# Performance work log

Measured on AMD Instinct MI355X. Metric: run time of the kernel, lower is better.

The kernel has to match this reference:

```python
import jax, jax.numpy as jnp
import numpy as np

B, L, T, V = 64, 512, 1000, 256
E, H, M, S = 256, 512, 80, 128  # text_embed, hidden, n_mels, speaker_dim


def lstm_scan(x, Wih, Whh, b):
    # x: [T, B, D]; torch gate order i, f, g, o; bias = b_ih + b_hh fused
    Bn = x.shape[1]
    Hn = Whh.shape[1]
    h0 = jnp.zeros((Bn, Hn), x.dtype)

    def step(carry, xt):
        h, c = carry
        g = xt @ Wih.T + h @ Whh.T + b
        i, f, gg, o = jnp.split(g, 4, axis=-1)
        c = jax.nn.sigmoid(f) * c + jax.nn.sigmoid(i) * jnp.tanh(gg)
        h = jax.nn.sigmoid(o) * jnp.tanh(c)
        return (h, c), h

    _, ys = jax.lax.scan(step, (h0, h0), x)
    return ys  # [T, B, H]


def setup_inputs() -> dict:
    key = jax.random.key(0)
    ks = jax.random.split(key, 32)
    r = lambda i, shp: (jax.random.normal(ks[i], shp, jnp.float32) * 0.1)
    Hd = H // 2  # 256, per-direction biLSTM hidden
    inp = {
        "text_input": jax.random.randint(ks[0], (B, L), 0, V),
        "speaker_embedding": jax.random.normal(ks[1], (B, S), jnp.float32),
        "target_mel": jax.random.normal(ks[2], (B, T, M), jnp.float32),
        "embed": r(3, (V, E)),
        # bidirectional text LSTM (hidden//2 per direction)
        "enc_Wih_f": r(4, (4 * Hd, E)), "enc_Whh_f": r(5, (4 * Hd, Hd)), "enc_b_f": r(6, (4 * Hd,)),
        "enc_Wih_b": r(7, (4 * Hd, E)), "enc_Whh_b": r(8, (4 * Hd, Hd)), "enc_b_b": r(9, (4 * Hd,)),
        # speaker projection MLP
        "sp_W1": r(10, (H, S)), "sp_b1": r(11, (H,)),
        "sp_W2": r(12, (H, H)), "sp_b2": r(13, (H,)),
        # 2-layer decoder LSTM, input = H + M = 592
        "dec_Wih0": r(14, (4 * H, H + M)), "dec_Whh0": r(15, (4 * H, H)), "dec_b0": r(16, (4 * H,)),
        "dec_Wih1": r(17, (4 * H, H)), "dec_Whh1": r(18, (4 * H, H)), "dec_b1": r(19, (4 * H,)),
        # mel projection MLP
        "mel_W1": r(20, (H, H)), "mel_b1": r(21, (H,)),
        "mel_W2": r(22, (M, H)), "mel_b2": r(23, (M,)),
        # stop token projection
        "stop_W": r(24, (1, H)), "stop_b": r(25, (1,)),
    }
    return inp


def reference(text_input, speaker_embedding, target_mel, embed,
              enc_Wih_f, enc_Whh_f, enc_b_f, enc_Wih_b, enc_Whh_b, enc_b_b,
              sp_W1, sp_b1, sp_W2, sp_b2,
              dec_Wih0, dec_Whh0, dec_b0, dec_Wih1, dec_Whh1, dec_b1,
              mel_W1, mel_b1, mel_W2, mel_b2, stop_W, stop_b):
    # --- text encoder: embedding + biLSTM ---
    x = jnp.swapaxes(embed[text_input], 0, 1)  # [L, B, E]
    fwd = lstm_scan(x, enc_Wih_f, enc_Whh_f, enc_b_f)          # [L, B, H/2]
    bwd = lstm_scan(x[::-1], enc_Wih_b, enc_Whh_b, enc_b_b)[::-1]
    text_encoded = jnp.swapaxes(jnp.concatenate([fwd, bwd], -1), 0, 1)  # [B, L, H]

    # --- speaker projection, broadcast over text length ---
    sp = jax.nn.relu(speaker_embedding @ sp_W1.T + sp_b1) @ sp_W2.T + sp_b2  # [B, H]
    encoder_output = text_encoded + sp[:, None, :]  # [B, L, H]

    # --- teacher-forced decoder: query_t = encoder_output[:, t % L] ---
    idx = jnp.arange(T) % L
    query = encoder_output[:, idx]  # [B, T, H]
    dec_mel_in = jnp.concatenate(
        [jnp.zeros((B, 1, M), target_mel.dtype), target_mel[:, :-1]], axis=1)  # [B, T, M]
    rnn_in = jnp.swapaxes(jnp.concatenate([dec_mel_in, query], -1), 0, 1)  # [T, B, H+M]

    h1 = lstm_scan(rnn_in, dec_Wih0, dec_Whh0, dec_b0)  # [T, B, H]
    h2 = lstm_scan(h1, dec_Wih1, dec_Whh1, dec_b1)      # [T, B, H]
    out = jnp.swapaxes(h2, 0, 1)  # [B, T, H]

    mel_outputs = jax.nn.relu(out @ mel_W1.T + mel_b1) @ mel_W2.T + mel_b2  # [B, T, M]
    stop_outputs = out @ stop_W.T + stop_b  # [B, T, 1]
    return mel_outputs, stop_outputs
```

## Files before the change

### kernel.cpp

```cpp
#include <hip/hip_runtime.h>
#include <cstdint>
#include <cstddef>


#define DEVI __device__ __forceinline__

typedef short bf16x8 __attribute__((ext_vector_type(8)));
typedef float f32x4 __attribute__((ext_vector_type(4)));
typedef unsigned short u16x4 __attribute__((ext_vector_type(4)));

constexpr int B_ = 64, L_ = 512, T_ = 1000, E_ = 256, H_ = 512, M_ = 80, S_ = 128, Hd_ = 256;

DEVI unsigned short f2bs(float f) {
  unsigned u = __builtin_bit_cast(unsigned, f);
  unsigned r = u + 0x7fffu + ((u >> 16) & 1u);
  return (unsigned short)(r >> 16);
}
DEVI float b2f(unsigned short s) { return __builtin_bit_cast(float, (unsigned)s << 16); }
DEVI void split2(float v, unsigned short& hi, unsigned short& lo) {
  hi = f2bs(v);
  lo = f2bs(v - b2f(hi));
}
DEVI float sigm(float x) { x = fminf(fmaxf(x, -30.f), 30.f); return 1.f / (1.f + __expf(-x)); }
DEVI float tanh_(float x) { x = fminf(fmaxf(x, -15.f), 15.f); float e = __expf(2.f * x); return (e - 1.f) / (e + 1.f); }

DEVI f32x4 mfma16(bf16x8 a, bf16x8 b, f32x4 c) {
  return __builtin_amdgcn_mfma_f32_16x16x32_bf16(a, b, c, 0, 0, 0);
}

DEVI void ldc16(bf16x8& r, const unsigned short* p) {
  asm volatile("global_load_dwordx4 %0, %1, off sc0 sc1" : "=v"(r) : "v"(p));
}
DEVI void st4c(unsigned short* p, unsigned v) {
  asm volatile("global_store_dword %0, %1, off sc0 sc1" :: "v"(p), "v"(v));
}
DEVI void st8c(unsigned short* p, u16x4 v) {
  asm volatile("global_store_dwordx2 %0, %1, off sc0 sc1" :: "v"(p), "v"(v));
}
DEVI int pollld(const int* p) {
  int v;
  asm volatile("global_load_dword %0, %1, off sc0 sc1\ns_waitcnt vmcnt(0)"
               : "=v"(v) : "v"(p) : "memory");
  return v;
}
#define VM_DRAIN() do { asm volatile("s_waitcnt vmcnt(0)" ::: "memory"); \
                        __builtin_amdgcn_sched_barrier(0); } while (0)
#define VM_WAIT8_OR_0(LAST) do { \
    if (LAST) asm volatile("s_waitcnt vmcnt(0)" ::: "memory"); \
    else      asm volatile("s_waitcnt vmcnt(8)" ::: "memory"); \
    __builtin_amdgcn_sched_barrier(0); } while (0)

struct Bar { int sub[8][64]; int master[64]; int release[64]; };

DEVI void grid_bar(Bar* bb, int nwg, int step) {
  __syncthreads();
  if (threadIdx.x == 0) {
    const int per = nwg >> 3;
    int old = __hip_atomic_fetch_add(&bb->sub[blockIdx.x & 7][0], 1,
                                     __ATOMIC_RELAXED, __HIP_MEMORY_SCOPE_AGENT);
    if (old == per * (step + 1) - 1) {
      int om = __hip_atomic_fetch_add(&bb->master[0], 1,
                                      __ATOMIC_RELAXED, __HIP_MEMORY_SCOPE_AGENT);
      if (om == 8 * (step + 1) - 1)
        __hip_atomic_fetch_add(&bb->release[0], 1,
                               __ATOMIC_RELAXED, __HIP_MEMORY_SCOPE_AGENT);
    }
    while (pollld(&bb->release[0]) < step + 1) __builtin_amdgcn_s_sleep(1);
  }
  __syncthreads();
}

__global__ void k_prep(const float* __restrict__ embed, const float* __restrict__ tmel,
                       const float* __restrict__ mw1, const float* __restrict__ mw2,
                       unsigned short* emb_h, unsigned short* emb_l,
                       unsigned short* mel_h, unsigned short* mel_l,
                       unsigned short* w1_bf, unsigned short* w2_bf) {
  const long long stride = (long long)gridDim.x * blockDim.x;
  const long long i0 = (long long)blockIdx.x * blockDim.x + threadIdx.x;
  for (long long i = i0; i < 256 * 256; i += stride) {
    unsigned short h, l; split2(embed[i], h, l);
    emb_h[i] = h; emb_l[i] = l;
  }
  for (long long i = i0; i < (long long)T_ * B_ * 96; i += stride) {
    int c = (int)(i % 96);
    long long tb = i / 96;
    int b = (int)(tb % B_);
    int t = (int)(tb / B_);
    float v = 0.f;
    if (t > 0 && c < 80) v = tmel[((long long)b * T_ + (t - 1)) * M_ + c];
    unsigned short h, l; split2(v, h, l);
    mel_h[i] = h; mel_l[i] = l;
  }
  for (long long i = i0; i < 512 * 512; i += stride) w1_bf[i] = f2bs(mw1[i]);
  for (long long i = i0; i < 80 * 512; i += stride) w2_bf[i] = f2bs(mw2[i]);
}

__global__ void __launch_bounds__(512) k_sp(const float* __restrict__ spk,
                                            const float* __restrict__ w1, const float* __restrict__ b1,
                                            const float* __restrict__ w2, const float* __restrict__ b2,
                                            float* sp) {
  __shared__ float t1[512];
  const int b = blockIdx.x, j = threadIdx.x;
  float a = b1[j];
  const float* sr = spk + b * S_;
  for (int k = 0; k < S_; ++k) a += sr[k] * w1[j * S_ + k];
  t1[j] = fmaxf(a, 0.f);
  __syncthreads();
  float a2 = b2[j];
  for (int k = 0; k < H_; ++k) a2 += t1[k] * w2[j * H_ + k];
  sp[b * H_ + j] = a2;
}

constexpr int ENC_LDS = 2 * 16 * 4 * 64 * 16 + 4 * 64 * 16 * 4 + 256;

__global__ void __launch_bounds__(256) k_enc(
    const int* __restrict__ text,
    const float* __restrict__ WihF, const float* __restrict__ WhhF, const float* __restrict__ bF,
    const float* __restrict__ WihB, const float* __restrict__ WhhB, const float* __restrict__ bB,
    const unsigned short* __restrict__ emb_h, const unsigned short* __restrict__ emb_l,
    const float* __restrict__ sp,
    unsigned short* hencfh, unsigned short* hencfl,
    unsigned short* ench, unsigned short* encl, Bar* bar) {
  extern __shared__ char lds[];
  unsigned short* Wh = (unsigned short*)lds;
  unsigned short* Wl = Wh + 16 * 4 * 64 * 8;
  float* G = (float*)(lds + 2 * 16 * 4 * 64 * 16);
  float* bias = G + 4 * 64 * 16;

  const int wg = blockIdx.x;
  const int dir = wg >> 4;
  const int jhb = (wg & 15) * 16;
  const int tid = threadIdx.x;
  const int wv = tid >> 6, ln = tid & 63, lg = ln >> 4, lr = ln & 15;

  const float* Wih = dir ? WihB : WihF;
  const float* Whh = dir ? WhhB : WhhF;
  const float* bb = dir ? bB : bF;

  for (int s = tid; s < 16 * 4 * 64; s += 256) {
    int kb = s >> 8, g = (s >> 6) & 3, l = s & 63;
    int R = g * Hd_ + jhb + (l & 15);
    int k0 = kb * 32 + (l >> 4) * 8;
    const float* src = (k0 < E_) ? (Wih + (size_t)R * E_ + k0) : (Whh + (size_t)R * Hd_ + (k0 - E_));
    bf16x8 vh, vl;
#pragma unroll
    for (int j = 0; j < 8; ++j) {
      unsigned short a, b; split2(src[j], a, b);
      vh[j] = (short)a; vl[j] = (short)b;
    }
    *(bf16x8*)(Wh + (size_t)s * 8) = vh;
    *(bf16x8*)(Wl + (size_t)s * 8) = vl;
  }
  if (tid < 64) bias[tid] = bb[(tid >> 4) * Hd_ + jhb + (tid & 15)];

  const int eb = tid >> 2, ej0 = (tid & 3) * 4;
  float c4[4] = {0.f, 0.f, 0.f, 0.f};
  float spv[4];
#pragma unroll
  for (int q = 0; q < 4; ++q) spv[q] = sp[eb * H_ + dir * Hd_ + jhb + ej0 + q];

  const int jh = jhb + ej0;
  const size_t fro = ((size_t)((jh >> 5) * 4 + (eb >> 4)) * 64 +
                      (((jh >> 3) & 3) * 16 + (eb & 15))) * 8 + (jh & 7);

  __syncthreads();

  for (int t = 0; t < L_; ++t) {
    const int tpos = dir ? (L_ - 1 - t) : t;
    const unsigned short* hsh = hencfh + ((size_t)((t & 1) * 2 + dir)) * 16384;
    const unsigned short* hsl = hencfl + ((size_t)((t & 1) * 2 + dir)) * 16384;
    unsigned short* hdh = hencfh + ((size_t)(((t + 1) & 1) * 2 + dir)) * 16384;
    unsigned short* hdl = hencfl + ((size_t)(((t + 1) & 1) * 2 + dir)) * 16384;

    for (int i = tid; i < 4096; i += 256) G[i] = bias[((i >> 10) << 4) + (i & 15)];

    int tix[4];
#pragma unroll
    for (int m = 0; m < 4; ++m) tix[m] = text[(16 * m + lr) * L_ + tpos];

    f32x4 acc[4][4];
#pragma unroll
    for (int g = 0; g < 4; ++g)
#pragma unroll
      for (int m = 0; m < 4; ++m) acc[g][m] = (f32x4){0.f, 0.f, 0.f, 0.f};

    auto MFE = [&](int kb, bf16x8 (&ah)[4], bf16x8 (&al)[4]) {
#pragma unroll
      for (int g = 0; g < 4; ++g) {
        bf16x8 bh = *(bf16x8*)(Wh + ((size_t)(kb * 4 + g) * 64 + ln) * 8);
        bf16x8 bl = *(bf16x8*)(Wl + ((size_t)(kb * 4 + g) * 64 + ln) * 8);
#pragma unroll
        for (int m = 0; m < 4; ++m) {
          acc[g][m] = mfma16(ah[m], bh, acc[g][m]);
          acc[g][m] = mfma16(al[m], bh, acc[g][m]);
          acc[g][m] = mfma16(ah[m], bl, acc[g][m]);
        }
      }
    };

    for (int kb = wv; kb < 8; kb += 4) {
      int k0 = kb * 32 + lg * 8;
      bf16x8 ah[4], al[4];
#pragma unroll
      for (int m = 0; m < 4; ++m) {
        ah[m] = *(const bf16x8*)(emb_h + (size_t)tix[m] * E_ + k0);
        al[m] = *(const bf16x8*)(emb_l + (size_t)tix[m] * E_ + k0);
      }
      MFE(kb, ah, al);
    }
    {
      auto issueE = [&](int kb, bf16x8 (&ah)[4], bf16x8 (&al)[4]) {
        const unsigned short* ph = hsh + ((size_t)((kb - 8) * 4) * 64 + ln) * 8;
        const unsigned short* pl = hsl + ((size_t)((kb - 8) * 4) * 64 + ln) * 8;
#pragma unroll
        for (int m = 0; m < 4; ++m) { ldc16(ah[m], ph + m * 512); ldc16(al[m], pl + m * 512); }
      };
      bf16x8 A0h[4], A0l[4], A1h[4], A1l[4];
      issueE(8 + wv, A0h, A0l);
      issueE(12 + wv, A1h, A1l);
      VM_WAIT8_OR_0(false);
      MFE(8 + wv, A0h, A0l);
      VM_WAIT8_OR_0(true);
      MFE(12 + wv, A1h, A1l);
    }

    __syncthreads();
#pragma unroll
    for (int g = 0; g < 4; ++g)
#pragma unroll
      for (int m = 0; m < 4; ++m)
#pragma unroll
        for (int r = 0; r < 4; ++r)
          atomicAdd(&G[(g * 64 + 16 * m + 4 * lg + r) * 16 + lr], acc[g][m][r]);
    __syncthreads();

    {
      u16x4 hvh, hvl, ovh, ovl;
#pragma unroll
      for (int q = 0; q < 4; ++q) {
        int jj = ej0 + q;
        float gi = G[(0 * 64 + eb) * 16 + jj];
        float gf = G[(1 * 64 + eb) * 16 + jj];
        float gg = G[(2 * 64 + eb) * 16 + jj];
        float go = G[(3 * 64 + eb) * 16 + jj];
        float cn = sigm(gf) * c4[q] + sigm(gi) * tanh_(gg);
        c4[q] = cn;
        float h = sigm(go) * tanh_(cn);
        unsigned short a, b; split2(h, a, b);
        hvh[q] = a; hvl[q] = b;
        float o = h + spv[q];
        split2(o, a, b);
        ovh[q] = a; ovl[q] = b;
      }
      st8c(hdh + fro, hvh);
      st8c(hdl + fro, hvl);
      *(u16x4*)(ench + ((size_t)eb * L_ + tpos) * H_ + dir * Hd_ + jhb + ej0) = ovh;
      *(u16x4*)(encl + ((size_t)eb * L_ + tpos) * H_ + dir * Hd_ + jhb + ej0) = ovl;
    }
    VM_DRAIN();
    grid_bar(bar, 32, t);
  }
}

constexpr int DEC_LDS = 2 * 35 * 2 * 64 * 16 + 4 * 64 * 8 * 4 + 128;

__global__ void __launch_bounds__(256) k_dec(
    const float* __restrict__ Wih0, const float* __restrict__ Whh0, const float* __restrict__ b0,
    const float* __restrict__ Wih1, const float* __restrict__ Whh1, const float* __restrict__ b1,
    const unsigned short* __restrict__ ench, const unsigned short* __restrict__ encl,
    const unsigned short* __restrict__ melh, const unsigned short* __restrict__ mell,
    unsigned short* h0fh, unsigned short* h0fl,
    unsigned short* h1fh, unsigned short* h1fl,
    unsigned short* h2_full, Bar* bar) {
  extern __shared__ char lds[];
  const int wg = blockIdx.x;
  const int layer = wg >> 6;
  const int jcb = (wg & 63) * 8;
  const int tid = threadIdx.x, wv = tid >> 6, ln = tid & 63, lg = ln >> 4, lr = ln & 15;
  const int NKB = layer ? 32 : 35;
  unsigned short* Wh = (unsigned short*)lds;
  unsigned short* Wl = Wh + (size_t)NKB * 2 * 64 * 8;
  float* G = (float*)(lds + (size_t)2 * NKB * 2 * 64 * 16);
  float* bias = G + 4 * 64 * 8;

  if (layer == 0) {
    for (int s = tid; s < 35 * 2 * 64; s += 256) {
      int kb = s >> 7, st = (s >> 6) & 1, l = s & 63;
      int n = l & 15;
      int R = (2 * st + (n >> 3)) * H_ + jcb + (n & 7);
      int k0 = kb * 32 + (l >> 4) * 8;
      bf16x8 vh, vl;
      if (k0 < 96) {
#pragma unroll
        for (int j = 0; j < 8; ++j) {
          int c = k0 + j;
          float v = (c < 80) ? Wih0[(size_t)R * 592 + c] : 0.f;
          unsigned short a, b; split2(v, a, b);
          vh[j] = (short)a; vl[j] = (short)b;
        }
      } else if (k0 < 608) {
        const float* src = Wih0 + (size_t)R * 592 + (k0 - 16);
#pragma unroll
        for (int j = 0; j < 8; ++j) {
          unsigned short a, b; split2(src[j], a, b);
          vh[j] = (short)a; vl[j] = (short)b;
        }
      } else {
        const float* src = Whh0 + (size_t)R * H_ + (k0 - 608);
#pragma unroll
        for (int j = 0; j < 8; ++j) {
          unsigned short a, b; split2(src[j], a, b);
          vh[j] = (short)a; vl[j] = (short)b;
        }
      }
      *(bf16x8*)(Wh + (size_t)s * 8) = vh;
      *(bf16x8*)(Wl + (size_t)s * 8) = vl;
    }
    if (tid < 32) bias[tid] = b0[(tid >> 3) * H_ + jcb + (tid & 7)];
  } else {
    for (int s = tid; s < 32 * 2 * 64; s += 256) {
      int kb = s >> 7, st = (s >> 6) & 1, l = s & 63;
      int n = l & 15;
      int R = (2 * st + (n >> 3)) * H_ + jcb + (n & 7);
      int k0 = kb * 32 + (l >> 4) * 8;
      const float* src = (k0 < 512) ? (Wih1 + (size_t)R * H_ + k0) : (Whh1 + (size_t)R * H_ + (k0 - 512));
      bf16x8 vh, vl;
#pragma unroll
      for (int j = 0; j < 8; ++j) {
        unsigned short a, b; split2(src[j], a, b);
        vh[j] = (short)a; vl[j] = (short)b;
      }
      *(bf16x8*)(Wh + (size_t)s * 8) = vh;
      *(bf16x8*)(Wl + (size_t)s * 8) = vl;
    }
    if (tid < 32) bias[tid] = b1[(tid >> 3) * H_ + jcb + (tid & 7)];
  }

  const int ebd = tid & 63, cc0 = (tid >> 6) * 2;
  float c2[2] = {0.f, 0.f};
  const int j0w = jcb + cc0;
  const size_t frw = ((size_t)((j0w >> 5) * 4 + (ebd >> 4)) * 64 +
                      (((j0w >> 3) & 3) * 16 + (ebd & 15))) * 8 + (j0w & 7);
  __syncthreads();

  for (int tau = 0; tau <= T_; ++tau) {
    const bool active = (layer == 0) ? (tau < T_) : (tau >= 1);
    if (active) {
      const int t = (layer == 0) ? tau : tau - 1;
      for (int i = tid; i < 2048; i += 256) G[i] = bias[((i >> 9) << 3) + (i & 7)];

      f32x4 acc[2][4];
#pragma unroll
      for (int st = 0; st < 2; ++st)
#pragma unroll
        for (int m = 0; m < 4; ++m) acc[st][m] = (f32x4){0.f, 0.f, 0.f, 0.f};

      auto MF = [&](int kb, bf16x8 (&ah)[4], bf16x8 (&al)[4]) {
#pragma unroll
        for (int st = 0; st < 2; ++st) {
          bf16x8 bh = *(bf16x8*)(Wh + ((size_t)(kb * 2 + st) * 64 + ln) * 8);
          bf16x8 bl = *(bf16x8*)(Wl + ((size_t)(kb * 2 + st) * 64 + ln) * 8);
#pragma unroll
          for (int m = 0; m < 4; ++m) {
            acc[st][m] = mfma16(ah[m], bh, acc[st][m]);
            acc[st][m] = mfma16(al[m], bh, acc[st][m]);
            acc[st][m] = mfma16(ah[m], bl, acc[st][m]);
          }
        }
      };

      if (layer == 0) {
        const int tq = t & (L_ - 1);
        const unsigned short* p0h = h0fh + (size_t)((tau + 1) & 1) * 32768;
        const unsigned short* p0l = h0fl + (size_t)((tau + 1) & 1) * 32768;
        for (int kb = wv; kb < 19; kb += 4) {
          int k0 = kb * 32 + lg * 8;
          bf16x8 ah[4], al[4];
          if (kb < 3) {
#pragma unroll
            for (int m = 0; m < 4; ++m) {
              ah[m] = *(const bf16x8*)(melh + ((size_t)t * B_ + 16 * m + lr) * 96 + k0);
              al[m] = *(const bf16x8*)(mell + ((size_t)t * B_ + 16 * m + lr) * 96 + k0);
            }
          } else {
            int k = k0 - 96;
#pragma unroll
            for (int m = 0; m < 4; ++m) {
              ah[m] = *(const bf16x8*)(ench + ((size_t)(16 * m + lr) * L_ + tq) * H_ + k);
              al[m] = *(const bf16x8*)(encl + ((size_t)(16 * m + lr) * L_ + tq) * H_ + k);
            }
          }
          MF(kb, ah, al);
        }
        {
          auto issue0 = [&](int kb, bf16x8 (&ah)[4], bf16x8 (&al)[4]) {
            const unsigned short* ph = p0h + ((size_t)((kb - 19) * 4) * 64 + ln) * 8;
            const unsigned short* pl = p0l + ((size_t)((kb - 19) * 4) * 64 + ln) * 8;
#pragma unroll
            for (int m = 0; m < 4; ++m) { ldc16(ah[m], ph + m * 512); ldc16(al[m], pl + m * 512); }
          };
          const int hkb0 = 19 + ((wv + 1) & 3);
          bf16x8 A0h[4], A0l[4], A1h[4], A1l[4];
          issue0(hkb0, A0h, A0l);
#pragma unroll
          for (int j = 0; j < 4; ++j) {
            const int kb = hkb0 + 4 * j;
            if (j & 1) {
              if (j < 3) issue0(kb + 4, A0h, A0l);
              VM_WAIT8_OR_0(j == 3);
              MF(kb, A1h, A1l);
            } else {
              if (j < 3) issue0(kb + 4, A1h, A1l);
              VM_WAIT8_OR_0(j == 3);
              MF(kb, A0h, A0l);
            }
          }
        }
      } else {
        const unsigned short* q0h = h0fh + (size_t)((tau + 1) & 1) * 32768;
        const unsigned short* q0l = h0fl + (size_t)((tau + 1) & 1) * 32768;
        const unsigned short* q1h = h1fh + (size_t)(tau & 1) * 32768;
        const unsigned short* q1l = h1fl + (size_t)(tau & 1) * 32768;
        auto issue1 = [&](int kb, bf16x8 (&ah)[4], bf16x8 (&al)[4]) {
          const unsigned short* ph = (kb < 16) ? (q0h + ((size_t)(kb * 4) * 64 + ln) * 8)
                                               : (q1h + ((size_t)((kb - 16) * 4) * 64 + ln) * 8);
          const unsigned short* pl = (kb < 16) ? (q0l + ((size_t)(kb * 4) * 64 + ln) * 8)
                                               : (q1l + ((size_t)((kb - 16) * 4) * 64 + ln) * 8);
#pragma unroll
          for (int m = 0; m < 4; ++m) { ldc16(ah[m], ph + m * 512); ldc16(al[m], pl + m * 512); }
        };
        bf16x8 A0h[4], A0l[4], A1h[4], A1l[4];
        issue1(wv, A0h, A0l);
#pragma unroll
        for (int i = 0; i < 8; ++i) {
          const int kb = wv + 4 * i;
          if (i & 1) {
            if (i < 7) issue1(kb + 4, A0h, A0l);
            VM_WAIT8_OR_0(i == 7);
            MF(kb, A1h, A1l);
          } else {
            if (i < 7) issue1(kb + 4, A1h, A1l);
            VM_WAIT8_OR_0(i == 7);
            MF(kb, A0h, A0l);
          }
        }
      }
      __syncthreads();
#pragma unroll
      for (int st = 0; st < 2; ++st)
#pragma unroll
        for (int m = 0; m < 4; ++m)
#pragma unroll
          for (int r = 0; r < 4; ++r) {
            int g = 2 * st + (lr >> 3), col = lr & 7;
            atomicAdd(&G[(g * 64 + 16 * m + 4 * lg + r) * 8 + col], acc[st][m][r]);
          }
      __syncthreads();

      {
        unsigned short* dh = layer ? (h1fh + (size_t)((tau + 1) & 1) * 32768)
                                   : (h0fh + (size_t)(tau & 1) * 32768);
        unsigned short* dl = layer ? (h1fl + (size_t)((tau + 1) & 1) * 32768)
                                   : (h0fl + (size_t)(tau & 1) * 32768);
        unsigned short hh[2], hl[2];
#pragma unroll
        for (int q = 0; q < 2; ++q) {
          int c = cc0 + q;
          float gi = G[(0 * 64 + ebd) * 8 + c];
          float gf = G[(1 * 64 + ebd) * 8 + c];
          float gg = G[(2 * 64 + ebd) * 8 + c];
          float go = G[(3 * 64 + ebd) * 8 + c];
          float cn = sigm(gf) * c2[q] + sigm(gi) * tanh_(gg);
          c2[q] = cn;
          float h = sigm(go) * tanh_(cn);
          split2(h, hh[q], hl[q]);
        }
        unsigned ph = (unsigned)hh[0] | ((unsigned)hh[1] << 16);
        unsigned pl = (unsigned)hl[0] | ((unsigned)hl[1] << 16);
        st4c(dh + frw, ph);
        st4c(dl + frw, pl);
        if (layer) *(unsigned*)(h2_full + ((size_t)t * B_ + ebd) * H_ + jcb + cc0) = ph;
      }
      VM_DRAIN();
    }
    grid_bar(bar, 128, tau);
  }
}

constexpr int MLP_LDS = 64 * 1024;

__global__ void __launch_bounds__(256) k_mlp(
    const unsigned short* __restrict__ h2_full,
    const unsigned short* __restrict__ w1_bf, const unsigned short* __restrict__ w2_bf,
    const float* __restrict__ mb1, const float* __restrict__ mb2,
    const float* __restrict__ stW, const float* __restrict__ stb, float* out) {
  extern __shared__ char lds[];
  const int t = blockIdx.x;
  const int tid = threadIdx.x, wv = tid >> 6, ln = tid & 63, lg = ln >> 4, lr = ln & 15;
  const unsigned short* A = h2_full + (size_t)t * B_ * H_;

  for (int half = 0; half < 2; ++half) {
    const int nb = wv * 8 + half * 4;
    f32x4 acc[4][4];
#pragma unroll
    for (int nn = 0; nn < 4; ++nn) {
      float bv = mb1[(nb + nn) * 16 + lr];
#pragma unroll
      for (int m = 0; m < 4; ++m) acc[m][nn] = (f32x4){bv, bv, bv, bv};
    }
    for (int kb = 0; kb < 16; ++kb) {
      int k0 = kb * 32 + lg * 8;
      bf16x8 afr[4], bfr[4];
#pragma unroll
      for (int m = 0; m < 4; ++m) afr[m] = *(const bf16x8*)(A + (size_t)(16 * m + lr) * H_ + k0);
#pragma unroll
      for (int nn = 0; nn < 4; ++nn) bfr[nn] = *(const bf16x8*)(w1_bf + (size_t)((nb + nn) * 16 + lr) * H_ + k0);
#pragma unroll
      for (int m = 0; m < 4; ++m)
#pragma unroll
        for (int nn = 0; nn < 4; ++nn) acc[m][nn] = mfma16(afr[m], bfr[nn], acc[m][nn]);
    }
#pragma unroll
    for (int m = 0; m < 4; ++m)
#pragma unroll
      for (int nn = 0; nn < 4; ++nn)
#pragma unroll
        for (int r = 0; r < 4; ++r) {
          int row = 16 * m + 4 * lg + r, col = (nb + nn) * 16 + lr;
          *(unsigned short*)(lds + row * 1024 + ((col * 2) ^ ((row & 7) << 4))) =
              f2bs(fmaxf(acc[m][nn][r], 0.f));
        }
  }
  __syncthreads();

  {
    f32x4 acc2[5];
#pragma unroll
    for (int n = 0; n < 5; ++n) {
      float bv = mb2[n * 16 + lr];
      acc2[n] = (f32x4){bv, bv, bv, bv};
    }
    for (int kb = 0; kb < 16; ++kb) {
      int k0 = kb * 32 + lg * 8;
      int row = 16 * wv + lr;
      bf16x8 afr = *(bf16x8*)(lds + row * 1024 + ((k0 * 2) ^ ((row & 7) << 4)));
#pragma unroll
      for (int n = 0; n < 5; ++n) {
        bf16x8 bfr = *(const bf16x8*)(w2_bf + (size_t)(n * 16 + lr) * H_ + k0);
        acc2[n] = mfma16(afr, bfr, acc2[n]);
      }
    }
#pragma unroll
    for (int n = 0; n < 5; ++n)
#pragma unroll
      for (int r = 0; r < 4; ++r) {
        int b = 16 * wv + 4 * lg + r;
        out[((size_t)b * T_ + t) * M_ + n * 16 + lr] = acc2[n][r];
      }
  }

  if (tid < 64) {
    int b = tid;
    float s = stb[0];
    const unsigned short* hp = A + (size_t)b * H_;
    for (int k = 0; k < H_; ++k) s += b2f(hp[k]) * stW[k];
    out[(size_t)B_ * T_ * M_ + (size_t)b * T_ + t] = s;
  }
}

extern "C" void kernel_launch(void* const* d_in, const int* in_sizes, int n_in,
                              void* d_out, int out_size, void* d_ws, size_t ws_size,
                              hipStream_t stream) {
  (void)in_sizes; (void)n_in; (void)out_size; (void)ws_size;
  const int* text = (const int*)d_in[0];
  const float* spk = (const float*)d_in[1];
  const float* tmel = (const float*)d_in[2];
  const float* embed = (const float*)d_in[3];
  const float* eWihF = (const float*)d_in[4];
  const float* eWhhF = (const float*)d_in[5];
  const float* ebF = (const float*)d_in[6];
  const float* eWihB = (const float*)d_in[7];
  const float* eWhhB = (const float*)d_in[8];
  const float* ebB = (const float*)d_in[9];
  const float* spW1 = (const float*)d_in[10];
  const float* spb1 = (const float*)d_in[11];
  const float* spW2 = (const float*)d_in[12];
  const float* spb2 = (const float*)d_in[13];
  const float* dWih0 = (const float*)d_in[14];
  const float* dWhh0 = (const float*)d_in[15];
  const float* db0 = (const float*)d_in[16];
  const float* dWih1 = (const float*)d_in[17];
  const float* dWhh1 = (const float*)d_in[18];
  const float* db1 = (const float*)d_in[19];
  const float* mW1 = (const float*)d_in[20];
  const float* mb1 = (const float*)d_in[21];
  const float* mW2 = (const float*)d_in[22];
  const float* mb2 = (const float*)d_in[23];
  const float* stW = (const float*)d_in[24];
  const float* stb = (const float*)d_in[25];
  float* out = (float*)d_out;

  char* base = (char*)d_ws;
  size_t off = 0;
  auto carve = [&](size_t bytes) -> void* {
    void* p = base + off;
    off += (bytes + 255) & ~(size_t)255;
    return p;
  };
  Bar* barE = (Bar*)carve(sizeof(Bar));
  Bar* barD = (Bar*)carve(sizeof(Bar));
  unsigned short* h0fh = (unsigned short*)carve((size_t)2 * 32768 * 2);
  unsigned short* h0fl = (unsigned short*)carve((size_t)2 * 32768 * 2);
  unsigned short* h1fh = (unsigned short*)carve((size_t)2 * 32768 * 2);
  unsigned short* h1fl = (unsigned short*)carve((size_t)2 * 32768 * 2);
  unsigned short* hencfh = (unsigned short*)carve((size_t)4 * 16384 * 2);
  unsigned short* hencfl = (unsigned short*)carve((size_t)4 * 16384 * 2);
  const size_t state_bytes = off;
  float* sp = (float*)carve((size_t)B_ * H_ * 4);
  unsigned short* emb_h = (unsigned short*)carve((size_t)256 * 256 * 2);
  unsigned short* emb_l = (unsigned short*)carve((size_t)256 * 256 * 2);
  unsigned short* mel_h = (unsigned short*)carve((size_t)T_ * B_ * 96 * 2);
  unsigned short* mel_l = (unsigned short*)carve((size_t)T_ * B_ * 96 * 2);
  unsigned short* w1_bf = (unsigned short*)carve((size_t)512 * 512 * 2);
  unsigned short* w2_bf = (unsigned short*)carve((size_t)80 * 512 * 2);
  unsigned short* ench = (unsigned short*)carve((size_t)B_ * L_ * H_ * 2);
  unsigned short* encl = (unsigned short*)carve((size_t)B_ * L_ * H_ * 2);
  unsigned short* h2_full = (unsigned short*)carve((size_t)T_ * B_ * H_ * 2);

  hipMemsetAsync(d_ws, 0, state_bytes, stream);

  hipFuncSetAttribute((const void*)k_enc, hipFuncAttributeMaxDynamicSharedMemorySize, ENC_LDS);
  hipFuncSetAttribute((const void*)k_dec, hipFuncAttributeMaxDynamicSharedMemorySize, DEC_LDS);
  hipFuncSetAttribute((const void*)k_mlp, hipFuncAttributeMaxDynamicSharedMemorySize, MLP_LDS);

  k_prep<<<2048, 256, 0, stream>>>(embed, tmel, mW1, mW2, emb_h, emb_l, mel_h, mel_l, w1_bf, w2_bf);
  k_sp<<<64, 512, 0, stream>>>(spk, spW1, spb1, spW2, spb2, sp);
  k_enc<<<32, 256, ENC_LDS, stream>>>(text, eWihF, eWhhF, ebF, eWihB, eWhhB, ebB,
                                      emb_h, emb_l, sp, hencfh, hencfl, ench, encl, barE);
  k_dec<<<128, 256, DEC_LDS, stream>>>(dWih0, dWhh0, db0, dWih1, dWhh1, db1,
                                       ench, encl, mel_h, mel_l,
                                       h0fh, h0fl, h1fh, h1fl, h2_full, barD);
  k_mlp<<<1000, 256, MLP_LDS, stream>>>(h2_full, w1_bf, w2_bf, mb1, mb2, stW, stb, out);
}
```

Before: 34.66 ms.

## Triple-buffer MFMA operand loads and use per-block release flags in grid barrier

Replaces the two-buffer load/compute loops in the encoder and decoder recurrent kernels with a generic three-stage software pipeline. The input-projection loads (embeddings, mel, encoder output) are now issued asynchronously and overlapped with MFMA work instead of being synchronous loads. The grid barrier is reworked to use 16 sub-counters and per-block release flags written by the last arriver, so each block polls its own cache line rather than one shared word. Launch bounds are set to one block per CU. The aim is to hide global-load latency and cut barrier contention in the per-timestep critical path, at the cost of more registers and a release fan-out store step.

Result: no change. 35.09 ms (+1.2%).

```diff
diff --git a/kernel.cpp b/kernel.cpp
--- a/kernel.cpp
+++ b/kernel.cpp
@@ -28,10 +28,16 @@
   return __builtin_amdgcn_mfma_f32_16x16x32_bf16(a, b, c, 0, 0, 0);
 }
 
+DEVI void ldg16(bf16x8& r, const unsigned short* p) {
+  asm volatile("global_load_dwordx4 %0, %1, off" : "=v"(r) : "v"(p));
+}
 DEVI void ldc16(bf16x8& r, const unsigned short* p) {
   asm volatile("global_load_dwordx4 %0, %1, off sc0 sc1" : "=v"(r) : "v"(p));
 }
 DEVI void st4c(unsigned short* p, unsigned v) {
+  asm volatile("global_store_dword %0, %1, off sc0 sc1" :: "v"(p), "v"(v));
+}
+DEVI void sti4c(int* p, int v) {
   asm volatile("global_store_dword %0, %1, off sc0 sc1" :: "v"(p), "v"(v));
 }
 DEVI void st8c(unsigned short* p, u16x4 v) {
@@ -43,31 +49,50 @@
                : "=v"(v) : "v"(p) : "memory");
   return v;
 }
-#define VM_DRAIN() do { asm volatile("s_waitcnt vmcnt(0)" ::: "memory"); \
-                        __builtin_amdgcn_sched_barrier(0); } while (0)
-#define VM_WAIT8_OR_0(LAST) do { \
-    if (LAST) asm volatile("s_waitcnt vmcnt(0)" ::: "memory"); \
-    else      asm volatile("s_waitcnt vmcnt(8)" ::: "memory"); \
-    __builtin_amdgcn_sched_barrier(0); } while (0)
-
-struct Bar { int sub[8][64]; int master[64]; int release[64]; };
-
-DEVI void grid_bar(Bar* bb, int nwg, int step) {
+#define WAITV(N) do { asm volatile("s_waitcnt vmcnt(" #N ")" ::: "memory"); \
+                      __builtin_amdgcn_sched_barrier(0); } while (0)
+#define VM_DRAIN() WAITV(0)
+
+struct Bar { int sub[16][16]; int master[16]; int rel[128][16]; };
+
+template <int NWG, int NSUB>
+DEVI void grid_barX(Bar* bb, int step) {
+  __shared__ int finS;
+  const int tid = threadIdx.x;
   __syncthreads();
-  if (threadIdx.x == 0) {
-    const int per = nwg >> 3;
-    int old = __hip_atomic_fetch_add(&bb->sub[blockIdx.x & 7][0], 1,
+  if (tid == 0) {
+    finS = 0;
+    constexpr int per = NWG / NSUB;
+    int old = __hip_atomic_fetch_add(&bb->sub[(int)blockIdx.x % NSUB][0], 1,
                                      __ATOMIC_RELAXED, __HIP_MEMORY_SCOPE_AGENT);
     if (old == per * (step + 1) - 1) {
       int om = __hip_atomic_fetch_add(&bb->master[0], 1,
                                       __ATOMIC_RELAXED, __HIP_MEMORY_SCOPE_AGENT);
-      if (om == 8 * (step + 1) - 1)
-        __hip_atomic_fetch_add(&bb->release[0], 1,
-                               __ATOMIC_RELAXED, __HIP_MEMORY_SCOPE_AGENT);
-    }
-    while (pollld(&bb->release[0]) < step + 1) __builtin_amdgcn_s_sleep(1);
+      if (om == NSUB * (step + 1) - 1) finS = 1;
+    }
   }
   __syncthreads();
+  if (finS && tid < NWG) sti4c(&bb->rel[tid][0], step + 1);
+  if (tid == 0) {
+    while (pollld(&bb->rel[(int)blockIdx.x][0]) < step + 1)
+      __builtin_amdgcn_s_sleep(1);
+  }
+  __syncthreads();
+}
+
+template <int N, class FI, class FM>
+DEVI void pipe3(FI issue, FM domf) {
+  bf16x8 S0[8], S1[8], S2[8];
+  issue(0, S0);
+  if constexpr (N > 1) issue(1, S1);
+  if constexpr (N > 2) issue(2, S2);
+#pragma unroll
+  for (int j = 0; j < N; ++j) {
+    if (j + 2 < N) { WAITV(16); } else if (j + 1 < N) { WAITV(8); } else { WAITV(0); }
+    if (j % 3 == 0)      { domf(j, S0); if (j + 3 < N) issue(j + 3, S0); }
+    else if (j % 3 == 1) { domf(j, S1); if (j + 3 < N) issue(j + 3, S1); }
+    else                 { domf(j, S2); if (j + 3 < N) issue(j + 3, S2); }
+  }
 }
 
 __global__ void k_prep(const float* __restrict__ embed, const float* __restrict__ tmel,
@@ -113,7 +138,7 @@
 
 constexpr int ENC_LDS = 2 * 16 * 4 * 64 * 16 + 4 * 64 * 16 * 4 + 256;
 
-__global__ void __launch_bounds__(256) k_enc(
+__global__ void __launch_bounds__(256, 1) k_enc(
     const int* __restrict__ text,
     const float* __restrict__ WihF, const float* __restrict__ WhhF, const float* __restrict__ bF,
     const float* __restrict__ WihB, const float* __restrict__ WhhB, const float* __restrict__ bB,
@@ -184,45 +209,37 @@
 #pragma unroll
       for (int m = 0; m < 4; ++m) acc[g][m] = (f32x4){0.f, 0.f, 0.f, 0.f};
 
-    auto MFE = [&](int kb, bf16x8 (&ah)[4], bf16x8 (&al)[4]) {
+    auto issue = [&](int j, bf16x8 (&S)[8]) {
+      const int kb = wv + 4 * j;
+      if (kb < 8) {
+        const int k0 = kb * 32 + lg * 8;
+#pragma unroll
+        for (int m = 0; m < 4; ++m) {
+          ldg16(S[m],     emb_h + (size_t)tix[m] * E_ + k0);
+          ldg16(S[4 + m], emb_l + (size_t)tix[m] * E_ + k0);
+        }
+      } else {
+        const unsigned short* ph = hsh + ((size_t)((kb - 8) * 4) * 64 + ln) * 8;
+        const unsigned short* pl = hsl + ((size_t)((kb - 8) * 4) * 64 + ln) * 8;
+#pragma unroll
+        for (int m = 0; m < 4; ++m) { ldc16(S[m], ph + m * 512); ldc16(S[4 + m], pl + m * 512); }
+      }
+    };
+    auto domf = [&](int j, bf16x8 (&S)[8]) {
+      const int kb = wv + 4 * j;
 #pragma unroll
       for (int g = 0; g < 4; ++g) {
         bf16x8 bh = *(bf16x8*)(Wh + ((size_t)(kb * 4 + g) * 64 + ln) * 8);
         bf16x8 bl = *(bf16x8*)(Wl + ((size_t)(kb * 4 + g) * 64 + ln) * 8);
 #pragma unroll
         for (int m = 0; m < 4; ++m) {
-          acc[g][m] = mfma16(ah[m], bh, acc[g][m]);
-          acc[g][m] = mfma16(al[m], bh, acc[g][m]);
-          acc[g][m] = mfma16(ah[m], bl, acc[g][m]);
+          acc[g][m] = mfma16(S[m],     bh, acc[g][m]);
+          acc[g][m] = mfma16(S[4 + m], bh, acc[g][m]);
+          acc[g][m] = mfma16(S[m],     bl, acc[g][m]);
         }
       }
     };
-
-    for (int kb = wv; kb < 8; kb += 4) {
-      int k0 = kb * 32 + lg * 8;
-      bf16x8 ah[4], al[4];
-#pragma unroll
-      for (int m = 0; m < 4; ++m) {
-        ah[m] = *(const bf16x8*)(emb_h + (size_t)tix[m] * E_ + k0);
-        al[m] = *(const bf16x8*)(emb_l + (size_t)tix[m] * E_ + k0);
-      }
-      MFE(kb, ah, al);
-    }
-    {
-      auto issueE = [&](int kb, bf16x8 (&ah)[4], bf16x8 (&al)[4]) {
-        const unsigned short* ph = hsh + ((size_t)((kb - 8) * 4) * 64 + ln) * 8;
-        const unsigned short* pl = hsl + ((size_t)((kb - 8) * 4) * 64 + ln) * 8;
-#pragma unroll
-        for (int m = 0; m < 4; ++m) { ldc16(ah[m], ph + m * 512); ldc16(al[m], pl + m * 512); }
-      };
-      bf16x8 A0h[4], A0l[4], A1h[4], A1l[4];
-      issueE(8 + wv, A0h, A0l);
-      issueE(12 + wv, A1h, A1l);
-      VM_WAIT8_OR_0(false);
-      MFE(8 + wv, A0h, A0l);
-      VM_WAIT8_OR_0(true);
-      MFE(12 + wv, A1h, A1l);
-    }
+    pipe3<4>(issue, domf);
 
     __syncthreads();
 #pragma unroll
@@ -258,13 +275,13 @@
       *(u16x4*)(encl + ((size_t)eb * L_ + tpos) * H_ + dir * Hd_ + jhb + ej0) = ovl;
     }
     VM_DRAIN();
-    grid_bar(bar, 32, t);
+    grid_barX<32, 8>(bar, t);
   }
 }
 
 constexpr int DEC_LDS = 2 * 35 * 2 * 64 * 16 + 4 * 64 * 8 * 4 + 128;
 
-__global__ void __launch_bounds__(256) k_dec(
+__global__ void __launch_bounds__(256, 1) k_dec(
     const float* __restrict__ Wih0, const float* __restrict__ Whh0, const float* __restrict__ b0,
     const float* __restrict__ Wih1, const float* __restrict__ Whh1, const float* __restrict__ b1,
     const unsigned short* __restrict__ ench, const unsigned short* __restrict__ encl,
@@ -355,16 +372,16 @@
 #pragma unroll
         for (int m = 0; m < 4; ++m) acc[st][m] = (f32x4){0.f, 0.f, 0.f, 0.f};
 
-      auto MF = [&](int kb, bf16x8 (&ah)[4], bf16x8 (&al)[4]) {
+      auto MF = [&](int kb, bf16x8 (&S)[8]) {
 #pragma unroll
         for (int st = 0; st < 2; ++st) {
           bf16x8 bh = *(bf16x8*)(Wh + ((size_t)(kb * 2 + st) * 64 + ln) * 8);
           bf16x8 bl = *(bf16x8*)(Wl + ((size_t)(kb * 2 + st) * 64 + ln) * 8);
 #pragma unroll
           for (int m = 0; m < 4; ++m) {
-            acc[st][m] = mfma16(ah[m], bh, acc[st][m]);
-            acc[st][m] = mfma16(al[m], bh, acc[st][m]);
-            acc[st][m] = mfma16(ah[m], bl, acc[st][m]);
+            acc[st][m] = mfma16(S[m],     bh, acc[st][m]);
+            acc[st][m] = mfma16(S[4 + m], bh, acc[st][m]);
+            acc[st][m] = mfma16(S[m],     bl, acc[st][m]);
           }
         }
       };
@@ -373,78 +390,50 @@
         const int tq = t & (L_ - 1);
         const unsigned short* p0h = h0fh + (size_t)((tau + 1) & 1) * 32768;
         const unsigned short* p0l = h0fl + (size_t)((tau + 1) & 1) * 32768;
-        for (int kb = wv; kb < 19; kb += 4) {
-          int k0 = kb * 32 + lg * 8;
-          bf16x8 ah[4], al[4];
+        auto issue = [&](int j, bf16x8 (&S)[8]) {
+          const int kb = wv + 4 * j;
+          const int k0 = kb * 32 + lg * 8;
           if (kb < 3) {
 #pragma unroll
             for (int m = 0; m < 4; ++m) {
-              ah[m] = *(const bf16x8*)(melh + ((size_t)t * B_ + 16 * m + lr) * 96 + k0);
-              al[m] = *(const bf16x8*)(mell + ((size_t)t * B_ + 16 * m + lr) * 96 + k0);
+              ldg16(S[m],     melh + ((size_t)t * B_ + 16 * m + lr) * 96 + k0);
+              ldg16(S[4 + m], mell + ((size_t)t * B_ + 16 * m + lr) * 96 + k0);
+            }
+          } else if (kb < 19) {
+            const int k = k0 - 96;
+#pragma unroll
+            for (int m = 0; m < 4; ++m) {
+              ldg16(S[m],     ench + ((size_t)(16 * m + lr) * L_ + tq) * H_ + k);
+              ldg16(S[4 + m], encl + ((size_t)(16 * m + lr) * L_ + tq) * H_ + k);
             }
           } else {
-            int k = k0 - 96;
-#pragma unroll
-            for (int m = 0; m < 4; ++m) {
-              ah[m] = *(const bf16x8*)(ench + ((size_t)(16 * m + lr) * L_ + tq) * H_ + k);
-              al[m] = *(const bf16x8*)(encl + ((size_t)(16 * m + lr) * L_ + tq) * H_ + k);
-            }
-          }
-          MF(kb, ah, al);
-        }
-        {
-          auto issue0 = [&](int kb, bf16x8 (&ah)[4], bf16x8 (&al)[4]) {
             const unsigned short* ph = p0h + ((size_t)((kb - 19) * 4) * 64 + ln) * 8;
             const unsigned short* pl = p0l + ((size_t)((kb - 19) * 4) * 64 + ln) * 8;
 #pragma unroll
-            for (int m = 0; m < 4; ++m) { ldc16(ah[m], ph + m * 512); ldc16(al[m], pl + m * 512); }
-          };
-          const int hkb0 = 19 + ((wv + 1) & 3);
-          bf16x8 A0h[4], A0l[4], A1h[4], A1l[4];
-          issue0(hkb0, A0h, A0l);
-#pragma unroll
-          for (int j = 0; j < 4; ++j) {
-            const int kb = hkb0 + 4 * j;
-            if (j & 1) {
-              if (j < 3) issue0(kb + 4, A0h, A0l);
-              VM_WAIT8_OR_0(j == 3);
-              MF(kb, A1h, A1l);
-            } else {
-              if (j < 3) issue0(kb + 4, A1h, A1l);
-              VM_WAIT8_OR_0(j == 3);
-              MF(kb, A0h, A0l);
-            }
+            for (int m = 0; m < 4; ++m) { ldc16(S[m], ph + m * 512); ldc16(S[4 + m], pl + m * 512); }
           }
-        }
+        };
+        auto domf = [&](int j, bf16x8 (&S)[8]) { MF(wv + 4 * j, S); };
+        if (wv < 3) pipe3<9>(issue, domf);
+        else        pipe3<8>(issue, domf);
       } else {
         const unsigned short* q0h = h0fh + (size_t)((tau + 1) & 1) * 32768;
         const unsigned short* q0l = h0fl + (size_t)((tau + 1) & 1) * 32768;
         const unsigned short* q1h = h1fh + (size_t)(tau & 1) * 32768;
         const unsigned short* q1l = h1fl + (size_t)(tau & 1) * 32768;
-        auto issue1 = [&](int kb, bf16x8 (&ah)[4], bf16x8 (&al)[4]) {
+        auto issue = [&](int j, bf16x8 (&S)[8]) {
+          const int kb = wv + 4 * j;
           const unsigned short* ph = (kb < 16) ? (q0h + ((size_t)(kb * 4) * 64 + ln) * 8)
                                                : (q1h + ((size_t)((kb - 16) * 4) * 64 + ln) * 8);
           const unsigned short* pl = (kb < 16) ? (q0l + ((size_t)(kb * 4) * 64 + ln) * 8)
                                                : (q1l + ((size_t)((kb - 16) * 4) * 64 + ln) * 8);
 #pragma unroll
-          for (int m = 0; m < 4; ++m) { ldc16(ah[m], ph + m * 512); ldc16(al[m], pl + m * 512); }
+          for (int m = 0; m < 4; ++m) { ldc16(S[m], ph + m * 512); ldc16(S[4 + m], pl + m * 512); }
         };
-        bf16x8 A0h[4], A0l[4], A1h[4], A1l[4];
-        issue1(wv, A0h, A0l);
-#pragma unroll
-        for (int i = 0; i < 8; ++i) {
-          const int kb = wv + 4 * i;
-          if (i & 1) {
-            if (i < 7) issue1(kb + 4, A0h, A0l);
-            VM_WAIT8_OR_0(i == 7);
-            MF(kb, A1h, A1l);
-          } else {
-            if (i < 7) issue1(kb + 4, A1h, A1l);
-            VM_WAIT8_OR_0(i == 7);
-            MF(kb, A0h, A0l);
-          }
-        }
-      }
+        auto domf = [&](int j, bf16x8 (&S)[8]) { MF(wv + 4 * j, S); };
+        pipe3<8>(issue, domf);
+      }
+
       __syncthreads();
 #pragma unroll
       for (int st = 0; st < 2; ++st)
@@ -483,7 +472,7 @@
       }
       VM_DRAIN();
     }
-    grid_bar(bar, 128, tau);
+    grid_barX<128, 16>(bar, tau);
   }
 }
 
```
